# Optimization experiments

Hardware: AMD Instinct MI355X
Metric: run time of the kernel (lower is better)

The kernel has to match this reference:

```python
import jax, jax.numpy as jnp
import numpy as np

NEG = 1e12  # matches torch's -(1-mask)*1e12 masking constant


def _rope_pointer(qw, kw, mask2d):
    # qw, kw: [B, L, K, H]; mask2d: [B, L, L] bool
    B, L, K, H = qw.shape
    # sinusoidal position embedding, interleaved [sin0,cos0,sin1,cos1,...]
    inv_freq = jnp.power(jnp.float32(10000.0), -2.0 * jnp.arange(H // 2, dtype=jnp.float32) / H)
    ang = jnp.arange(L, dtype=jnp.float32)[:, None] * inv_freq  # [L, H/2]
    cos_pos = jnp.repeat(jnp.cos(ang), 2, axis=-1)[None, :, None, :]  # [1,L,1,H]
    sin_pos = jnp.repeat(jnp.sin(ang), 2, axis=-1)[None, :, None, :]

    def rot(x):
        x2 = jnp.stack([-x[..., 1::2], x[..., ::2]], axis=-1).reshape(x.shape)
        return x * cos_pos + x2 * sin_pos

    q = rot(qw)
    k = rot(kw)
    logits = jnp.einsum('bmhd,bnhd->bhmn', q, k)  # [B,K,L,L]
    m = mask2d[:, None, :, :].astype(logits.dtype)  # [B,1,L,L] broadcasts over K
    return logits * m - (1.0 - m) * NEG


def setup_inputs() -> dict:
    key = jax.random.key(0)
    ks = jax.random.split(key, 8)
    B, L, H = 16, 256, 1024
    tri_hid = arg_hid = eve_hid = 64
    role_num = 60
    scale = 1.0 / np.sqrt(H)
    inp = {
        'cond_bert_embs': jax.random.normal(ks[0], (B, L, H), jnp.float32),
        'tri_W': jax.random.normal(ks[1], (2 * tri_hid, H), jnp.float32) * scale,
        'tri_b': jax.random.normal(ks[2], (2 * tri_hid,), jnp.float32) * 0.01,
        'arg_W': jax.random.normal(ks[3], (2 * arg_hid, H), jnp.float32) * scale,
        'arg_b': jax.random.normal(ks[4], (2 * arg_hid,), jnp.float32) * 0.01,
        'role_W': jax.random.normal(ks[5], (2 * eve_hid * role_num, H), jnp.float32) * scale,
        'role_b': jax.random.normal(ks[6], (2 * eve_hid * role_num,), jnp.float32) * 0.01,
        'word_mask2d': jnp.ones((B, L, L), dtype=bool),
        'triu_mask2d': jnp.triu(jnp.ones((B, L, L), dtype=bool)),
    }
    return inp


def reference(cond_bert_embs, tri_W, tri_b, arg_W, arg_b, role_W, role_b,
              word_mask2d, triu_mask2d):
    B, L, H = cond_bert_embs.shape
    tri_hid = tri_W.shape[0] // 2
    arg_hid = arg_W.shape[0] // 2
    eve_hid = tri_hid  # eve_hid_size == tri_hid_size here
    role_num = role_W.shape[0] // (2 * eve_hid)

    # trigger pointer: K = 1 head
    tri_reps = (cond_bert_embs @ tri_W.T + tri_b).reshape(B, L, 1, 2 * tri_hid)
    tri_qw, tri_kw = jnp.split(tri_reps, 2, axis=-1)
    tri_logits = _rope_pointer(tri_qw, tri_kw, word_mask2d).transpose(0, 2, 3, 1)  # [B,L,L,1]

    # argument pointer: K = 1 head
    arg_reps = (cond_bert_embs @ arg_W.T + arg_b).reshape(B, L, 1, 2 * arg_hid)
    arg_qw, arg_kw = jnp.split(arg_reps, 2, axis=-1)
    arg_logits = _rope_pointer(arg_qw, arg_kw, word_mask2d).transpose(0, 2, 3, 1)  # [B,L,L,1]

    # role pointer: K = role_num heads, upper-triangular mask
    role_reps = (cond_bert_embs @ role_W.T + role_b).reshape(B, L, role_num, 2 * eve_hid)
    role_qw, role_kw = jnp.split(role_reps, 2, axis=-1)
    role_logits = _rope_pointer(role_qw, role_kw, triu_mask2d).transpose(0, 2, 3, 1)
    role_logits = role_logits.reshape(B, L, L, -1, role_num)  # [B,L,L,1,role_num]

    return (tri_logits, arg_logits, role_logits)
```

## Files before the change

kernel.cpp:

```cpp
#include <hip/hip_runtime.h>
#include <hip/hip_bf16.h>
#include <stdint.h>


typedef __attribute__((ext_vector_type(8)))  short short8;
typedef __attribute__((ext_vector_type(4)))  float f32x4;
typedef __attribute__((ext_vector_type(4)))  uint16_t u16x4;

#define LQ    256
#define HID   1024
#define NH    62
#define HSTR  16384
#define NEGF  (-1000727379968.0f)
#define TA_OFF   1048576ULL
#define ROLE_OFF 2097152ULL

__device__ __forceinline__ uint16_t f2bf(float x) {
  uint32_t u = __builtin_bit_cast(uint32_t, x);
  return (uint16_t)((u + 0x7FFFu + ((u >> 16) & 1u)) >> 16);
}
__device__ __forceinline__ uint16_t f2bf_tr(float x) {
  return (uint16_t)(__builtin_bit_cast(uint32_t, x) >> 16);
}
__device__ __forceinline__ float bf2f(uint16_t b) {
  uint32_t u = ((uint32_t)b) << 16;
  return __builtin_bit_cast(float, u);
}
__device__ __forceinline__ int mask_mode(const void* p) {
  uint32_t w0 = *(const uint32_t*)p;
  if (w0 == 0x01010101u) return 0;
  if (w0 == 1u)          return 1;
  if (w0 == 0x3F803F80u) return 2;
  return 3;
}
__device__ __forceinline__ bool mask_at(const void* p, int mode, size_t idx) {
  if (mode == 0) return ((const uint8_t*)p)[idx] != 0;
  if (mode == 1) return ((const int*)p)[idx] != 0;
  if (mode == 2) return (((const uint16_t*)p)[idx] & 0x7FFFu) != 0;
  return ((const float*)p)[idx] != 0.0f;
}
__device__ __forceinline__ void rope_cs(int pos, float invf, float* s, float* c) {
  float ang = (float)pos * invf;
  __sincosf(ang, s, c);
}
__device__ __forceinline__ float rope_invf(int p) {
  return exp2f(-(float)p * (13.287712379549449f / 32.0f));
}
__device__ __forceinline__ void gload16(const short* g, short* l) {
  __builtin_amdgcn_global_load_lds(
      (const __attribute__((address_space(1))) void*)g,
      (__attribute__((address_space(3))) void*)l, 16, 0, 0);
}

#define EGRP 524288
#define WGRP 1015808
__global__ __launch_bounds__(256)
void k_preconv(const float* __restrict__ E,
               const float* __restrict__ triW, const float* __restrict__ argW,
               const float* __restrict__ roleW,
               short* __restrict__ Eb, short* __restrict__ Wb) {
  for (int gid = blockIdx.x * 256 + threadIdx.x; gid < EGRP + WGRP;
       gid += gridDim.x * 256) {
    const float* src;
    short* dst;
    if (gid < EGRP) {
      int row = gid >> 7, col8 = gid & 127;
      src = E + (size_t)row * HID + col8 * 8;
      dst = Eb + (((size_t)(row >> 4)) * 32 + (col8 >> 2)) * 512
               + (row & 15) * 32 + (col8 & 3) * 8;
    } else {
      int g = gid - EGRP;
      int row = g >> 7, col8 = g & 127;
      const float* srow = (row < 128) ? triW + (size_t)row * HID
                        : (row < 256) ? argW + (size_t)(row - 128) * HID
                                      : roleW + (size_t)(row - 256) * HID;
      src = srow + col8 * 8;
      dst = Wb + (((size_t)(row >> 4)) * 32 + (col8 >> 2)) * 512
               + (row & 15) * 32 + (col8 & 3) * 8;
    }
    f32x4 v0 = *reinterpret_cast<const f32x4*>(src);
    f32x4 v1 = *reinterpret_cast<const f32x4*>(src + 4);
    short8 r;
    r[0] = (short)f2bf_tr(v0[0]); r[1] = (short)f2bf_tr(v0[1]);
    r[2] = (short)f2bf_tr(v0[2]); r[3] = (short)f2bf_tr(v0[3]);
    r[4] = (short)f2bf_tr(v1[0]); r[5] = (short)f2bf_tr(v1[1]);
    r[6] = (short)f2bf_tr(v1[2]); r[7] = (short)f2bf_tr(v1[3]);
    *reinterpret_cast<short8*>(dst) = r;
  }
}

__global__ __launch_bounds__(256)
void k_proj_pre(const short* __restrict__ Eb, const short* __restrict__ Wb,
                const float* __restrict__ triB, const float* __restrict__ argB,
                const float* __restrict__ roleB,
                short* __restrict__ qs, short* __restrict__ ks, int b0) {
  const int nb = blockIdx.x;
  const int mb = blockIdx.y;
  const int n0 = nb * 128;
  const int mrow0 = b0 * LQ + mb * 128;
  const int lrow0 = mb * 128;

  const float* Bv;
  if (nb == 0)      Bv = triB;
  else if (nb == 1) Bv = argB;
  else              Bv = roleB + (n0 - 256);

  __shared__ short As[2][128 * 32];
  __shared__ short Bs[2][128 * 32];

  const int tid  = threadIdx.x;
  const int lane = tid & 63;
  const int w    = tid >> 6;
  const int wm   = (w >> 1) * 64, wn = (w & 1) * 64;
  const int l8   = lane * 8;
  const int mt0  = mrow0 >> 4;
  const int nt0  = n0 >> 4;

  f32x4 acc[4][4] = {};

  auto stage = [&](int buf, int kt) {
#pragma unroll
    for (int cc = 0; cc < 2; ++cc) {
      const int c = w * 2 + cc;
      gload16(Eb + ((size_t)(mt0 + c) * 32 + kt) * 512 + l8, &As[buf][c * 512]);
      gload16(Wb + ((size_t)(nt0 + c) * 32 + kt) * 512 + l8, &Bs[buf][c * 512]);
    }
  };

  stage(0, 0);
  __syncthreads();
  for (int t = 0; t < 32; ++t) {
    const int buf = t & 1;
    if (t + 1 < 32) stage(buf ^ 1, t + 1);
    short8 af[4], bfr[4];
#pragma unroll
    for (int i = 0; i < 4; ++i)
      af[i] = *reinterpret_cast<const short8*>(
          &As[buf][(wm + i * 16 + (lane & 15)) * 32 + (lane >> 4) * 8]);
#pragma unroll
    for (int j = 0; j < 4; ++j)
      bfr[j] = *reinterpret_cast<const short8*>(
          &Bs[buf][(wn + j * 16 + (lane & 15)) * 32 + (lane >> 4) * 8]);
#pragma unroll
    for (int i = 0; i < 4; ++i)
#pragma unroll
      for (int j = 0; j < 4; ++j)
        acc[i][j] = __builtin_amdgcn_mfma_f32_16x16x32_bf16(af[i], bfr[j], acc[i][j], 0, 0, 0);
    __syncthreads();
  }

  const int col_l = lane & 15;
  const int row_h = (lane >> 4) * 4;
#pragma unroll
  for (int j = 0; j < 4; ++j) {
    const int n_loc = wn + j * 16 + col_l;
    const int gcol  = n0 + n_loc;
    const float bias = Bv[n_loc];
    const int d    = gcol & 63;
    const int head = gcol >> 7;
    const bool is_k = (gcol >> 6) & 1;
    const bool odd = d & 1;
    const float invf = rope_invf(d >> 1);
    short* dst = is_k ? ks : qs;
#pragma unroll
    for (int i = 0; i < 4; ++i) {
#pragma unroll
      for (int r = 0; r < 4; ++r) {
        float v  = acc[i][j][r] + bias;
        float vp = __shfl_xor(v, 1, 64);
        int tl  = lrow0 + wm + i * 16 + row_h + r;
        int pos = tl & (LQ - 1);
        float s, c;
        rope_cs(pos, invf, &s, &c);
        float o = odd ? (v * c + vp * s) : (v * c - vp * s);
        dst[((size_t)(tl >> 8) * NH + head) * HSTR + (size_t)pos * 64 + d] =
            (short)f2bf(o);
      }
    }
  }
}

__global__ __launch_bounds__(256)
void k_proj_chunk(const float* __restrict__ E,
                  const float* __restrict__ triW, const float* __restrict__ triB,
                  const float* __restrict__ argW, const float* __restrict__ argB,
                  const float* __restrict__ roleW, const float* __restrict__ roleB,
                  short* __restrict__ qs, short* __restrict__ ks, int b0) {
  const int nb = blockIdx.x;
  const int mb = blockIdx.y;
  const int n0 = nb * 128;
  const int mrow0 = b0 * LQ + mb * 128;
  const int lrow0 = mb * 128;

  const float* W;  const float* Bv;
  if (nb == 0)      { W = triW;                             Bv = triB; }
  else if (nb == 1) { W = argW;                             Bv = argB; }
  else              { W = roleW + (size_t)(n0 - 256) * HID; Bv = roleB + (n0 - 256); }

  __shared__ short As[2][128 * 32];
  __shared__ short Bs[2][128 * 32];

  const int tid  = threadIdx.x;
  const int lane = tid & 63;
  const int w    = tid >> 6;
  const int wm   = (w >> 1) * 64, wn = (w & 1) * 64;
  const int srow = tid >> 2;
  const int scol = (tid & 3) * 8;

  f32x4 acc[4][4] = {};
  f32x4 ra0[2], ra1[2], rb0[2], rb1[2];

  auto load_regs = [&](int k0) {
    const float* pa0 = E + (size_t)(mrow0 + srow) * HID + k0 + scol;
    const float* pa1 = E + (size_t)(mrow0 + 64 + srow) * HID + k0 + scol;
    const float* pb0 = W + (size_t)(srow) * HID + k0 + scol;
    const float* pb1 = W + (size_t)(64 + srow) * HID + k0 + scol;
    ra0[0] = *reinterpret_cast<const f32x4*>(pa0);
    ra0[1] = *reinterpret_cast<const f32x4*>(pa0 + 4);
    ra1[0] = *reinterpret_cast<const f32x4*>(pa1);
    ra1[1] = *reinterpret_cast<const f32x4*>(pa1 + 4);
    rb0[0] = *reinterpret_cast<const f32x4*>(pb0);
    rb0[1] = *reinterpret_cast<const f32x4*>(pb0 + 4);
    rb1[0] = *reinterpret_cast<const f32x4*>(pb1);
    rb1[1] = *reinterpret_cast<const f32x4*>(pb1 + 4);
  };
  auto cvt8 = [&](const f32x4* v) -> short8 {
    short8 r;
    r[0] = (short)f2bf_tr(v[0][0]); r[1] = (short)f2bf_tr(v[0][1]);
    r[2] = (short)f2bf_tr(v[0][2]); r[3] = (short)f2bf_tr(v[0][3]);
    r[4] = (short)f2bf_tr(v[1][0]); r[5] = (short)f2bf_tr(v[1][1]);
    r[6] = (short)f2bf_tr(v[1][2]); r[7] = (short)f2bf_tr(v[1][3]);
    return r;
  };
  auto write_lds = [&](int buf) {
    *reinterpret_cast<short8*>(&As[buf][srow * 32 + scol])        = cvt8(ra0);
    *reinterpret_cast<short8*>(&As[buf][(64 + srow) * 32 + scol]) = cvt8(ra1);
    *reinterpret_cast<short8*>(&Bs[buf][srow * 32 + scol])        = cvt8(rb0);
    *reinterpret_cast<short8*>(&Bs[buf][(64 + srow) * 32 + scol]) = cvt8(rb1);
  };

  load_regs(0); write_lds(0); __syncthreads();
  const int NT = HID / 32;
  for (int t = 0; t < NT; ++t) {
    if (t + 1 < NT) load_regs((t + 1) * 32);
    const int buf = t & 1;
    short8 af[4], bfr[4];
#pragma unroll
    for (int i = 0; i < 4; ++i)
      af[i] = *reinterpret_cast<const short8*>(
          &As[buf][(wm + i * 16 + (lane & 15)) * 32 + (lane >> 4) * 8]);
#pragma unroll
    for (int j = 0; j < 4; ++j)
      bfr[j] = *reinterpret_cast<const short8*>(
          &Bs[buf][(wn + j * 16 + (lane & 15)) * 32 + (lane >> 4) * 8]);
#pragma unroll
    for (int i = 0; i < 4; ++i)
#pragma unroll
      for (int j = 0; j < 4; ++j)
        acc[i][j] = __builtin_amdgcn_mfma_f32_16x16x32_bf16(af[i], bfr[j], acc[i][j], 0, 0, 0);
    __syncthreads();
    if (t + 1 < NT) { write_lds((t + 1) & 1); __syncthreads(); }
  }

  const int col_l = lane & 15;
  const int row_h = (lane >> 4) * 4;
#pragma unroll
  for (int j = 0; j < 4; ++j) {
    const int n_loc = wn + j * 16 + col_l;
    const int gcol  = n0 + n_loc;
    const float bias = Bv[n_loc];
    const int d    = gcol & 63;
    const int head = gcol >> 7;
    const bool is_k = (gcol >> 6) & 1;
    const bool odd = d & 1;
    const float invf = rope_invf(d >> 1);
    short* dst = is_k ? ks : qs;
#pragma unroll
    for (int i = 0; i < 4; ++i) {
#pragma unroll
      for (int r = 0; r < 4; ++r) {
        float v  = acc[i][j][r] + bias;
        float vp = __shfl_xor(v, 1, 64);
        int tl  = lrow0 + wm + i * 16 + row_h + r;
        int pos = tl & (LQ - 1);
        float s, c;
        rope_cs(pos, invf, &s, &c);
        float o = odd ? (v * c + vp * s) : (v * c - vp * s);
        dst[((size_t)(tl >> 8) * NH + head) * HSTR + (size_t)pos * 64 + d] =
            (short)f2bf(o);
      }
    }
  }
}

__global__ __launch_bounds__(512)
void k_role3(const short* __restrict__ qs, const short* __restrict__ ks,
             const void* __restrict__ triu_mask, float* __restrict__ out,
             int b0) {
  const int nt = blockIdx.x, mt = blockIdx.y, bz = blockIdx.z;
  const int bg = b0 + bz;
  const int m0 = mt * 16, n0 = nt * 32;
  __shared__ uint16_t tile[16 * 32 * 60];

  const int tid = threadIdx.x, lane = tid & 63, w = tid >> 6;
  const int frow = lane & 15;
  const int koff = (lane >> 4) * 8;
  const size_t cbase = (size_t)bz * NH;

  auto do_head = [&](int r) {
    const size_t hb = (cbase + 2 + r) * HSTR;
    short8 aq[2], bk[2][2];
#pragma unroll
    for (int kc = 0; kc < 2; ++kc) {
      aq[kc] = *reinterpret_cast<const short8*>(
          qs + hb + (size_t)(m0 + frow) * 64 + kc * 32 + koff);
      bk[0][kc] = *reinterpret_cast<const short8*>(
          ks + hb + (size_t)(n0 + frow) * 64 + kc * 32 + koff);
      bk[1][kc] = *reinterpret_cast<const short8*>(
          ks + hb + (size_t)(n0 + 16 + frow) * 64 + kc * 32 + koff);
    }
    f32x4 acc[2] = {};
#pragma unroll
    for (int jf = 0; jf < 2; ++jf)
#pragma unroll
      for (int kc = 0; kc < 2; ++kc)
        acc[jf] = __builtin_amdgcn_mfma_f32_16x16x32_bf16(aq[kc], bk[jf][kc], acc[jf], 0, 0, 0);
#pragma unroll
    for (int jf = 0; jf < 2; ++jf)
#pragma unroll
      for (int rg = 0; rg < 4; ++rg) {
        int m = (lane >> 4) * 4 + rg;
        int n = jf * 16 + (lane & 15);
        tile[(m * 32 + n) * 60 + r] = f2bf(acc[jf][rg]);
      }
  };

  if (w < 4) {
    const int h0 = w * 8;
#pragma unroll 2
    for (int i = 0; i < 8; ++i) do_head(h0 + i);
  } else {
    const int h0 = 32 + (w - 4) * 7;
#pragma unroll 2
    for (int i = 0; i < 7; ++i) do_head(h0 + i);
  }
  __syncthreads();

  const int mode = mask_mode(triu_mask);
  const size_t maskbase = ((size_t)bg * LQ + m0) * LQ + n0;
  const size_t outbase  = ROLE_OFF + (((size_t)bg * LQ + m0) * LQ + n0) * 60;
  for (int f = tid; f < 7680; f += 512) {
    int e  = f * 4;
    int m  = e / 1920;
    int x  = e - m * 1920;
    int n_ = x / 60;
    u16x4 tv = *reinterpret_cast<const u16x4*>(&tile[e]);
    bool mk = mask_at(triu_mask, mode, maskbase + (size_t)m * LQ + n_);
    f32x4 v;
    v[0] = mk ? bf2f(tv[0]) : NEGF;
    v[1] = mk ? bf2f(tv[1]) : NEGF;
    v[2] = mk ? bf2f(tv[2]) : NEGF;
    v[3] = mk ? bf2f(tv[3]) : NEGF;
    *reinterpret_cast<f32x4*>(&out[outbase + (size_t)m * (LQ * 60) + x]) = v;
  }
}

__global__ __launch_bounds__(256)
void k_ta_chunk(const short* __restrict__ qs, const short* __restrict__ ks,
                const void* __restrict__ word_mask, float* __restrict__ out,
                int b0) {
  const int mt = blockIdx.x, h = blockIdx.y, bz = blockIdx.z;
  const int bg = b0 + bz;
  const int m0 = mt * 32;
  __shared__ uint16_t tile[32 * 256];

  const int tid = threadIdx.x, lane = tid & 63, w = tid >> 6;
  const int frow = lane & 31;
  const int koff = (lane >> 5) * 8;
  const size_t hb = ((size_t)bz * NH + h) * HSTR;

  short8 aq[4];
#pragma unroll
  for (int kc = 0; kc < 4; ++kc)
    aq[kc] = *reinterpret_cast<const short8*>(
        qs + hb + (size_t)(m0 + frow) * 64 + kc * 16 + koff);

  typedef __attribute__((ext_vector_type(16))) float f32x16l;
#pragma unroll
  for (int jn = 0; jn < 2; ++jn) {
    const int ncol0 = w * 64 + jn * 32;
    short8 bk[4];
#pragma unroll
    for (int kc = 0; kc < 4; ++kc)
      bk[kc] = *reinterpret_cast<const short8*>(
          ks + hb + (size_t)(ncol0 + frow) * 64 + kc * 16 + koff);
    f32x16l acc = {};
#pragma unroll
    for (int kc = 0; kc < 4; ++kc)
      acc = __builtin_amdgcn_mfma_f32_32x32x16_bf16(aq[kc], bk[kc], acc, 0, 0, 0);
#pragma unroll
    for (int rg = 0; rg < 16; ++rg) {
      int m = (rg & 3) + 8 * (rg >> 2) + 4 * (lane >> 5);
      int n = ncol0 + (lane & 31);
      tile[m * 256 + n] = f2bf(acc[rg]);
    }
  }
  __syncthreads();

  const int mode = mask_mode(word_mask);
  const size_t maskbase = ((size_t)bg * LQ + m0) * LQ;
  const size_t outbase  = (size_t)h * TA_OFF + ((size_t)bg * LQ + m0) * LQ;
  for (int e = tid; e < 8192; e += 256) {
    int m = e >> 8, n = e & 255;
    bool mk = mask_at(word_mask, mode, maskbase + (size_t)m * LQ + n);
    out[outbase + e] = mk ? bf2f(tile[e]) : NEGF;
  }
}

__global__ __launch_bounds__(256)
void k_ta_fused(const float* __restrict__ E,
                const float* __restrict__ triW, const float* __restrict__ triB,
                const float* __restrict__ argW, const float* __restrict__ argB,
                const void* __restrict__ word_mask, float* __restrict__ out) {
  const int h = blockIdx.x, b = blockIdx.y;
  const float* W  = h ? argW : triW;
  const float* Bv = h ? argB : triB;

  __shared__ short As[2][128 * 32];
  __shared__ short Bs[2][128 * 32];
  __shared__ short qk[256 * 128];

  const int tid  = threadIdx.x;
  const int lane = tid & 63;
  const int w    = tid >> 6;
  const int wm   = (w >> 1) * 64, wn = (w & 1) * 64;
  const int srow = tid >> 2;
  const int scol = (tid & 3) * 8;
  const int col_l = lane & 15;
  const int row_h = (lane >> 4) * 4;

  for (int mi = 0; mi < 2; ++mi) {
    const int r0 = mi * 128;
    f32x4 acc[4][4] = {};
    f32x4 ra0[2], ra1[2], rb0[2], rb1[2];
    auto load_regs = [&](int k0) {
      const float* pa0 = E + ((size_t)b * LQ + r0 + srow) * HID + k0 + scol;
      const float* pa1 = E + ((size_t)b * LQ + r0 + 64 + srow) * HID + k0 + scol;
      const float* pb0 = W + (size_t)(srow) * HID + k0 + scol;
      const float* pb1 = W + (size_t)(64 + srow) * HID + k0 + scol;
      ra0[0] = *reinterpret_cast<const f32x4*>(pa0);
      ra0[1] = *reinterpret_cast<const f32x4*>(pa0 + 4);
      ra1[0] = *reinterpret_cast<const f32x4*>(pa1);
      ra1[1] = *reinterpret_cast<const f32x4*>(pa1 + 4);
      rb0[0] = *reinterpret_cast<const f32x4*>(pb0);
      rb0[1] = *reinterpret_cast<const f32x4*>(pb0 + 4);
      rb1[0] = *reinterpret_cast<const f32x4*>(pb1);
      rb1[1] = *reinterpret_cast<const f32x4*>(pb1 + 4);
    };
    auto cvt8 = [&](const f32x4* v) -> short8 {
      short8 r;
      r[0] = (short)f2bf_tr(v[0][0]); r[1] = (short)f2bf_tr(v[0][1]);
      r[2] = (short)f2bf_tr(v[0][2]); r[3] = (short)f2bf_tr(v[0][3]);
      r[4] = (short)f2bf_tr(v[1][0]); r[5] = (short)f2bf_tr(v[1][1]);
      r[6] = (short)f2bf_tr(v[1][2]); r[7] = (short)f2bf_tr(v[1][3]);
      return r;
    };
    auto write_lds = [&](int buf) {
      *reinterpret_cast<short8*>(&As[buf][srow * 32 + scol])        = cvt8(ra0);
      *reinterpret_cast<short8*>(&As[buf][(64 + srow) * 32 + scol]) = cvt8(ra1);
      *reinterpret_cast<short8*>(&Bs[buf][srow * 32 + scol])        = cvt8(rb0);
      *reinterpret_cast<short8*>(&Bs[buf][(64 + srow) * 32 + scol]) = cvt8(rb1);
    };
    load_regs(0); write_lds(0); __syncthreads();
    for (int t = 0; t < 32; ++t) {
      if (t + 1 < 32) load_regs((t + 1) * 32);
      const int buf = t & 1;
      short8 af[4], bfr[4];
#pragma unroll
      for (int i = 0; i < 4; ++i)
        af[i] = *reinterpret_cast<const short8*>(
            &As[buf][(wm + i * 16 + col_l) * 32 + (lane >> 4) * 8]);
#pragma unroll
      for (int j = 0; j < 4; ++j)
        bfr[j] = *reinterpret_cast<const short8*>(
            &Bs[buf][(wn + j * 16 + col_l) * 32 + (lane >> 4) * 8]);
#pragma unroll
      for (int i = 0; i < 4; ++i)
#pragma unroll
        for (int j = 0; j < 4; ++j)
          acc[i][j] = __builtin_amdgcn_mfma_f32_16x16x32_bf16(af[i], bfr[j], acc[i][j], 0, 0, 0);
      __syncthreads();
      if (t + 1 < 32) { write_lds((t + 1) & 1); __syncthreads(); }
    }
#pragma unroll
    for (int j = 0; j < 4; ++j) {
      const int n_loc = wn + j * 16 + col_l;
      const float bias = Bv[n_loc];
      const int d = n_loc & 63;
      const bool odd = d & 1;
      const float invf = rope_invf(d >> 1);
#pragma unroll
      for (int i = 0; i < 4; ++i) {
#pragma unroll
        for (int r = 0; r < 4; ++r) {
          float v  = acc[i][j][r] + bias;
          float vp = __shfl_xor(v, 1, 64);
          int pos = r0 + wm + i * 16 + row_h + r;
          float s, c;
          rope_cs(pos, invf, &s, &c);
          float o = odd ? (v * c + vp * s) : (v * c - vp * s);
          qk[pos * 128 + n_loc] = (short)f2bf(o);
        }
      }
    }
    __syncthreads();
  }

  const int mode = mask_mode(word_mask);
  short8 aq[4][2];
#pragma unroll
  for (int i = 0; i < 4; ++i)
#pragma unroll
    for (int kk = 0; kk < 2; ++kk)
      aq[i][kk] = *reinterpret_cast<const short8*>(
          &qk[(w * 64 + i * 16 + col_l) * 128 + kk * 32 + (lane >> 4) * 8]);

  for (int ncb = 0; ncb < 4; ++ncb) {
    const int nbase = ncb * 64;
    short8 bk[4][2];
#pragma unroll
    for (int j = 0; j < 4; ++j)
#pragma unroll
      for (int kk = 0; kk < 2; ++kk)
        bk[j][kk] = *reinterpret_cast<const short8*>(
            &qk[(nbase + j * 16 + col_l) * 128 + 64 + kk * 32 + (lane >> 4) * 8]);
    f32x4 acc[4][4] = {};
#pragma unroll
    for (int i = 0; i < 4; ++i)
#pragma unroll
      for (int j = 0; j < 4; ++j)
#pragma unroll
        for (int kk = 0; kk < 2; ++kk)
          acc[i][j] = __builtin_amdgcn_mfma_f32_16x16x32_bf16(aq[i][kk], bk[j][kk], acc[i][j], 0, 0, 0);
#pragma unroll
    for (int i = 0; i < 4; ++i)
#pragma unroll
      for (int j = 0; j < 4; ++j)
#pragma unroll
        for (int r = 0; r < 4; ++r) {
          int gm = w * 64 + i * 16 + row_h + r;
          int gn = nbase + j * 16 + col_l;
          size_t mi_ = ((size_t)b * LQ + gm) * LQ + gn;
          bool mk = mask_at(word_mask, mode, mi_);
          out[(size_t)h * TA_OFF + mi_] = mk ? acc[i][j][r] : NEGF;
        }
  }
}

extern "C" void kernel_launch(void* const* d_in, const int* in_sizes, int n_in,
                              void* d_out, int out_size, void* d_ws, size_t ws_size,
                              hipStream_t stream) {
  (void)in_sizes; (void)n_in; (void)out_size;
  const float* E     = (const float*)d_in[0];
  const float* triW  = (const float*)d_in[1];
  const float* triB  = (const float*)d_in[2];
  const float* argW  = (const float*)d_in[3];
  const float* argB  = (const float*)d_in[4];
  const float* roleW = (const float*)d_in[5];
  const float* roleB = (const float*)d_in[6];
  const void*  wmask = d_in[7];
  const void*  tmask = d_in[8];
  float* out = (float*)d_out;

  const size_t PER_B = (size_t)NH * HSTR * 2 * 2;
  const size_t PRE   = ((size_t)4096 * HID + (size_t)7936 * HID) * 2;

  int cb_pre = (ws_size > PRE) ? (int)((ws_size - PRE) / PER_B) : 0;
  if (cb_pre > 16) cb_pre = 16;

  if (cb_pre >= 1) {
    short* qs = (short*)d_ws;
    short* ks = qs + (size_t)cb_pre * NH * HSTR;
    short* Eb = ks + (size_t)cb_pre * NH * HSTR;
    short* Wb = Eb + (size_t)4096 * HID;
    k_preconv<<<dim3(2048), dim3(256), 0, stream>>>(E, triW, argW, roleW, Eb, Wb);
    for (int b0 = 0; b0 < 16; b0 += cb_pre) {
      int cbi = (16 - b0 < cb_pre) ? (16 - b0) : cb_pre;
      k_proj_pre<<<dim3(62, 2 * cbi), dim3(256), 0, stream>>>(
          Eb, Wb, triB, argB, roleB, qs, ks, b0);
      k_role3<<<dim3(8, 16, cbi), dim3(512), 0, stream>>>(qs, ks, tmask, out, b0);
      k_ta_chunk<<<dim3(8, 2, cbi), dim3(256), 0, stream>>>(qs, ks, wmask, out, b0);
    }
    return;
  }

  int cb = (int)(ws_size / PER_B);
  if (cb > 16) cb = 16;
  if (cb >= 1) {
    short* qs = (short*)d_ws;
    short* ks = qs + (size_t)cb * NH * HSTR;
    for (int b0 = 0; b0 < 16; b0 += cb) {
      int cbi = (16 - b0 < cb) ? (16 - b0) : cb;
      k_proj_chunk<<<dim3(62, 2 * cbi), dim3(256), 0, stream>>>(
          E, triW, triB, argW, argB, roleW, roleB, qs, ks, b0);
      k_role3<<<dim3(8, 16, cbi), dim3(512), 0, stream>>>(qs, ks, tmask, out, b0);
      k_ta_chunk<<<dim3(8, 2, cbi), dim3(256), 0, stream>>>(qs, ks, wmask, out, b0);
    }
  } else {
    short* qs = (short*)d_out;
    short* ks = qs + (size_t)NH * HSTR;
    for (int b0 = 0; b0 < 16; ++b0) {
      k_proj_chunk<<<dim3(62, 2), dim3(256), 0, stream>>>(
          E, triW, triB, argW, argB, roleW, roleB, qs, ks, b0);
      k_role3<<<dim3(8, 16, 1), dim3(512), 0, stream>>>(qs, ks, tmask, out, b0);
    }
    k_ta_fused<<<dim3(2, 16), dim3(256), 0, stream>>>(E, triW, triB, argW, argB,
                                                      wmask, out);
  }
}
```

Measured before the change: 269.9 us.

## Enlarge projection tile to a full batch row and use a precomputed RoPE table

The projection GEMM now uses 512-thread blocks that each cover a whole 256-row batch element against a 128-column weight tile. Each weight tile is therefore loaded once per batch instead of twice, while the LDS A-buffer doubles. The per-element sincos in the epilogue is replaced by a lookup into a cos/sin table built once by a new small kernel in the workspace. The cost is fewer, larger blocks (62 x cbi), which lowers grid parallelism, plus an extra launch and higher LDS use per block.

```diff
diff --git a/kernel.cpp b/kernel.cpp
--- a/kernel.cpp
+++ b/kernel.cpp
@@ -5,6 +5,7 @@
 
 typedef __attribute__((ext_vector_type(8)))  short short8;
 typedef __attribute__((ext_vector_type(4)))  float f32x4;
+typedef __attribute__((ext_vector_type(2)))  float f32x2;
 typedef __attribute__((ext_vector_type(4)))  uint16_t u16x4;
 
 #define LQ    256
@@ -50,6 +51,17 @@
   __builtin_amdgcn_global_load_lds(
       (const __attribute__((address_space(1))) void*)g,
       (__attribute__((address_space(3))) void*)l, 16, 0, 0);
+}
+
+__global__ __launch_bounds__(256)
+void k_tables(f32x2* __restrict__ tab) {
+  int t   = blockIdx.x * 256 + threadIdx.x;
+  int pos = t >> 5, p = t & 31;
+  float ang = (float)pos * rope_invf(p);
+  float s, c;
+  __sincosf(ang, &s, &c);
+  f32x2 v; v[0] = c; v[1] = s;
+  tab[t] = v;
 }
 
 #define EGRP 524288
@@ -89,29 +101,29 @@
   }
 }
 
-__global__ __launch_bounds__(256)
-void k_proj_pre(const short* __restrict__ Eb, const short* __restrict__ Wb,
-                const float* __restrict__ triB, const float* __restrict__ argB,
-                const float* __restrict__ roleB,
-                short* __restrict__ qs, short* __restrict__ ks, int b0) {
+__global__ __launch_bounds__(512)
+void k_proj2(const short* __restrict__ Eb, const short* __restrict__ Wb,
+             const float* __restrict__ triB, const float* __restrict__ argB,
+             const float* __restrict__ roleB, const f32x2* __restrict__ tab,
+             short* __restrict__ qs, short* __restrict__ ks, int b0) {
   const int nb = blockIdx.x;
   const int mb = blockIdx.y;
   const int n0 = nb * 128;
-  const int mrow0 = b0 * LQ + mb * 128;
-  const int lrow0 = mb * 128;
+  const int mrow0 = (b0 + mb) * LQ;
 
   const float* Bv;
   if (nb == 0)      Bv = triB;
   else if (nb == 1) Bv = argB;
   else              Bv = roleB + (n0 - 256);
 
-  __shared__ short As[2][128 * 32];
+  __shared__ short As[2][256 * 32];
   __shared__ short Bs[2][128 * 32];
 
   const int tid  = threadIdx.x;
   const int lane = tid & 63;
   const int w    = tid >> 6;
-  const int wm   = (w >> 1) * 64, wn = (w & 1) * 64;
+  const int wm   = (w >> 1) * 64;
+  const int wn   = (w & 1) * 64;
   const int l8   = lane * 8;
   const int mt0  = mrow0 >> 4;
   const int nt0  = n0 >> 4;
@@ -123,8 +135,8 @@
     for (int cc = 0; cc < 2; ++cc) {
       const int c = w * 2 + cc;
       gload16(Eb + ((size_t)(mt0 + c) * 32 + kt) * 512 + l8, &As[buf][c * 512]);
-      gload16(Wb + ((size_t)(nt0 + c) * 32 + kt) * 512 + l8, &Bs[buf][c * 512]);
-    }
+    }
+    gload16(Wb + ((size_t)(nt0 + w) * 32 + kt) * 512 + l8, &Bs[buf][w * 512]);
   };
 
   stage(0, 0);
@@ -160,7 +172,7 @@
     const int head = gcol >> 7;
     const bool is_k = (gcol >> 6) & 1;
     const bool odd = d & 1;
-    const float invf = rope_invf(d >> 1);
+    const int p    = d >> 1;
     short* dst = is_k ? ks : qs;
 #pragma unroll
     for (int i = 0; i < 4; ++i) {
@@ -168,12 +180,10 @@
       for (int r = 0; r < 4; ++r) {
         float v  = acc[i][j][r] + bias;
         float vp = __shfl_xor(v, 1, 64);
-        int tl  = lrow0 + wm + i * 16 + row_h + r;
-        int pos = tl & (LQ - 1);
-        float s, c;
-        rope_cs(pos, invf, &s, &c);
-        float o = odd ? (v * c + vp * s) : (v * c - vp * s);
-        dst[((size_t)(tl >> 8) * NH + head) * HSTR + (size_t)pos * 64 + d] =
+        int pos = wm + i * 16 + row_h + r;
+        f32x2 cs = tab[pos * 32 + p];
+        float o = odd ? (v * cs[0] + vp * cs[1]) : (v * cs[0] - vp * cs[1]);
+        dst[((size_t)mb * NH + head) * HSTR + (size_t)pos * 64 + d] =
             (short)f2bf(o);
       }
     }
@@ -573,7 +583,8 @@
   float* out = (float*)d_out;
 
   const size_t PER_B = (size_t)NH * HSTR * 2 * 2;
-  const size_t PRE   = ((size_t)4096 * HID + (size_t)7936 * HID) * 2;
+  const size_t PRE   = ((size_t)4096 * HID + (size_t)7936 * HID) * 2
+                     + 8192 * 8;
 
   int cb_pre = (ws_size > PRE) ? (int)((ws_size - PRE) / PER_B) : 0;
   if (cb_pre > 16) cb_pre = 16;
@@ -583,11 +594,13 @@
     short* ks = qs + (size_t)cb_pre * NH * HSTR;
     short* Eb = ks + (size_t)cb_pre * NH * HSTR;
     short* Wb = Eb + (size_t)4096 * HID;
+    f32x2* tab = (f32x2*)(Wb + (size_t)7936 * HID);
+    k_tables<<<dim3(32), dim3(256), 0, stream>>>(tab);
     k_preconv<<<dim3(2048), dim3(256), 0, stream>>>(E, triW, argW, roleW, Eb, Wb);
     for (int b0 = 0; b0 < 16; b0 += cb_pre) {
       int cbi = (16 - b0 < cb_pre) ? (16 - b0) : cb_pre;
-      k_proj_pre<<<dim3(62, 2 * cbi), dim3(256), 0, stream>>>(
-          Eb, Wb, triB, argB, roleB, qs, ks, b0);
+      k_proj2<<<dim3(62, cbi), dim3(512), 0, stream>>>(
+          Eb, Wb, triB, argB, roleB, tab, qs, ks, b0);
       k_role3<<<dim3(8, 16, cbi), dim3(512), 0, stream>>>(qs, ks, tmask, out, b0);
       k_ta_chunk<<<dim3(8, 2, cbi), dim3(256), 0, stream>>>(qs, ks, wmask, out, b0);
     }
```

Measured after the change: 298.6 us. 10.6% more time.
